# Optimization experiments

Hardware: AMD Instinct MI355X
Metric: run time of the kernel (lower is better)

The kernel has to match this reference:

```python
import jax, jax.numpy as jnp
import numpy as np

B, T, V_LEN = 64, 21, 36
E, H, F, VOC = 512, 512, 1024, 20000


def _gru_cell(x, h, w_ih, w_hh, b_ih, b_hh):
    # PyTorch nn.GRUCell semantics
    gi = x @ w_ih.T + b_ih            # (B, 3H)
    gh = h @ w_hh.T + b_hh            # (B, 3H)
    i_r, i_z, i_n = jnp.split(gi, 3, axis=1)
    h_r, h_z, h_n = jnp.split(gh, 3, axis=1)
    r = jax.nn.sigmoid(i_r + h_r)
    z = jax.nn.sigmoid(i_z + h_z)
    n = jnp.tanh(i_n + r * h_n)
    return (1.0 - z) * n + z * h


def setup_inputs() -> dict:
    key = jax.random.key(0)
    ks = jax.random.split(key, 20)

    def w(k, shape, fan_in):
        return jax.random.normal(k, shape, dtype=jnp.float32) * (1.0 / np.sqrt(fan_in))

    att_in = H + E + F   # h2_dim + input_dim + feature_dim
    lang_in = F + H      # feature_dim + h1_dim
    return {
        "feature_vector": jax.random.normal(ks[0], (B, V_LEN, F), dtype=jnp.float32),
        "ground_truth_seq_helper": T,
        "ground_truth_answer_input": jax.random.normal(ks[1], (B, T, E), dtype=jnp.float32),
        # attention GRUCell
        "att_w_ih": w(ks[2], (3 * H, att_in), att_in),
        "att_w_hh": w(ks[3], (3 * H, H), H),
        "att_b_ih": w(ks[4], (3 * H,), H),
        "att_b_hh": w(ks[5], (3 * H,), H),
        # language GRUCell
        "lang_w_ih": w(ks[6], (3 * H, lang_in), lang_in),
        "lang_w_hh": w(ks[7], (3 * H, H), H),
        "lang_b_ih": w(ks[8], (3 * H,), H),
        "lang_b_hh": w(ks[9], (3 * H,), H),
        # attention MLP
        "fc1_w": w(ks[10], (128, F), F),
        "fc1_b": w(ks[11], (128,), F),
        "fc2_w": w(ks[12], (128, H), H),
        "fc2_b": w(ks[13], (128,), H),
        "fc3_w": w(ks[14], (1, 128), 128),
        "fc3_b": w(ks[15], (1,), 128),
        # vocab projection
        "dense_w": w(ks[16], (VOC, H), H),
        "dense_b": w(ks[17], (VOC,), H),
    }


def reference(feature_vector, ground_truth_seq_helper, ground_truth_answer_input,
              att_w_ih, att_w_hh, att_b_ih, att_b_hh,
              lang_w_ih, lang_w_hh, lang_b_ih, lang_b_hh,
              fc1_w, fc1_b, fc2_w, fc2_b, fc3_w, fc3_b,
              dense_w, dense_b):
    batch = feature_vector.shape[0]
    v_mean = feature_vector.mean(axis=1)                     # (B, F) loop-invariant
    v_w = feature_vector @ fc1_w.T + fc1_b                   # (B, L, 128) loop-invariant

    def step(carry, x_t):
        h1, h2 = carry
        x = jnp.concatenate([h2, x_t, v_mean], axis=1)       # (B, H+E+F)
        h1 = _gru_cell(x, h1, att_w_ih, att_w_hh, att_b_ih, att_b_hh)
        h_w = h1 @ fc2_w.T + fc2_b                           # (B, 128)
        s = jnp.tanh(v_w + h_w[:, None, :]) @ fc3_w.T + fc3_b  # (B, L, 1)
        a = jax.nn.softmax(s[..., 0], axis=-1)               # (B, L)
        mix = jnp.einsum('bl,blf->bf', a, feature_vector)    # (B, F)
        h2 = _gru_cell(jnp.concatenate([mix, h1], axis=1), h2,
                       lang_w_ih, lang_w_hh, lang_b_ih, lang_b_hh)
        logits = h2 @ dense_w.T + dense_b                    # (B, VOC)
        return (h1, h2), logits

    h1 = jnp.zeros((batch, H), dtype=feature_vector.dtype)
    h2 = jnp.zeros((batch, H), dtype=feature_vector.dtype)
    xs = jnp.swapaxes(ground_truth_answer_input[:, :-1, :], 0, 1)  # (T-1, B, E)
    _, logits = jax.lax.scan(step, (h1, h2), xs)
    result = jnp.swapaxes(logits, 0, 1)                      # (B, T-1, VOC)
    return result
```

## Files before the change

### kernel.cpp

```cpp
#include <hip/hip_runtime.h>
#include <hip/hip_bf16.h>
#include <math.h>


typedef __attribute__((ext_vector_type(8))) short bf16x8;
typedef __attribute__((ext_vector_type(4))) float f32x4;
typedef unsigned short u16;
typedef unsigned int u32;

#define MFMA16 __builtin_amdgcn_mfma_f32_16x16x32_bf16

__device__ __forceinline__ u16 f2bf(float f){
  u32 u = __float_as_uint(f);
  u += 0x7fffu + ((u >> 16) & 1u);
  return (u16)(u >> 16);
}
__device__ __forceinline__ float bf2f(u16 u){ return __uint_as_float(((u32)u) << 16); }
__device__ __forceinline__ float sigm(float x){ return 1.0f/(1.0f+__expf(-x)); }

#define OFF_VMEAN  ((size_t)0)
#define OFF_VMW    ((size_t)262144)
#define OFF_VW     ((size_t)655360)
#define OFF_PREX   ((size_t)1835008)
#define OFF_GTBF   ((size_t)10092544)
#define OFF_WMIDBF ((size_t)11468800)
#define OFF_WIH2HI ((size_t)13041664)
#define OFF_WIH2LO ((size_t)14614528)
#define OFF_AWHHHI ((size_t)16187392)
#define OFF_AWHHLO ((size_t)17760256)
#define OFF_LWHHHI ((size_t)19333120)
#define OFF_LWHHLO ((size_t)20905984)
#define OFF_LWIHHI ((size_t)22478848)
#define OFF_LWIHLO ((size_t)27197440)
#define OFF_H1HI   ((size_t)31916032)
#define OFF_H1LO   ((size_t)32047104)
#define OFF_H2HI   ((size_t)32178176)
#define OFF_H2LO   ((size_t)32309248)
#define OFF_MIXHI  ((size_t)32440320)
#define OFF_MIXLO  ((size_t)32571392)
#define OFF_G2F    ((size_t)32702464)
#define OFF_GHH2F  ((size_t)33095680)
#define OFF_H2BF   ((size_t)33488896)
#define OFF_WDBF   ((size_t)0)

__global__ __launch_bounds__(256) void k_prep0(
    const float* __restrict__ fv, const float* __restrict__ gt,
    const float* __restrict__ awih, const float* __restrict__ awhh,
    const float* __restrict__ lwih, const float* __restrict__ lwhh,
    char* __restrict__ ws){
  long gid = (long)blockIdx.x * blockDim.x + threadIdx.x;
  long stride = (long)gridDim.x * blockDim.x;
  u32* zh1h = (u32*)(ws + OFF_H1HI);
  u32* zh1l = (u32*)(ws + OFF_H1LO);
  u32* zh2h = (u32*)(ws + OFF_H2HI);
  u32* zh2l = (u32*)(ws + OFF_H2LO);
  for (long i = gid; i < 16384; i += stride){ zh1h[i]=0; zh1l[i]=0; zh2h[i]=0; zh2l[i]=0; }
  u16* gtbf = (u16*)(ws + OFF_GTBF);
  for (long i = gid; i < 688128; i += stride) gtbf[i] = f2bf(gt[i]);
  u16* wmid = (u16*)(ws + OFF_WMIDBF);
  for (long i = gid; i < 786432; i += stride)
    wmid[i] = f2bf(awih[(i>>9)*2048 + 512 + (i&511)]);
  u16* w2h = (u16*)(ws + OFF_WIH2HI); u16* w2l = (u16*)(ws + OFF_WIH2LO);
  for (long i = gid; i < 786432; i += stride){
    float x = awih[(i>>9)*2048 + (i&511)];
    u16 h = f2bf(x); w2h[i] = h; w2l[i] = f2bf(x - bf2f(h));
  }
  u16* ahh = (u16*)(ws + OFF_AWHHHI); u16* ahl = (u16*)(ws + OFF_AWHHLO);
  for (long i = gid; i < 786432; i += stride){
    float x = awhh[i]; u16 h = f2bf(x); ahh[i] = h; ahl[i] = f2bf(x - bf2f(h));
  }
  u16* lhh = (u16*)(ws + OFF_LWHHHI); u16* lhl = (u16*)(ws + OFF_LWHHLO);
  for (long i = gid; i < 786432; i += stride){
    float x = lwhh[i]; u16 h = f2bf(x); lhh[i] = h; lhl[i] = f2bf(x - bf2f(h));
  }
  u16* lih = (u16*)(ws + OFF_LWIHHI); u16* lil = (u16*)(ws + OFF_LWIHLO);
  for (long i = gid; i < 2359296; i += stride){
    float x = lwih[i]; u16 h = f2bf(x); lih[i] = h; lil[i] = f2bf(x - bf2f(h));
  }
  float* vmean = (float*)(ws + OFF_VMEAN);
  for (long i = gid; i < 65536; i += stride){
    long b = i >> 10, f = i & 1023;
    float s = 0.f;
    for (int l = 0; l < 36; ++l) s += fv[b*36864 + l*1024 + f];
    vmean[i] = s * (1.f/36.f);
  }
}

__global__ __launch_bounds__(256) void k_prep1(const float* __restrict__ fv,
    const float* __restrict__ att_w_ih, const float* __restrict__ att_b_ih,
    const float* __restrict__ fc1_w, const float* __restrict__ fc1_b,
    char* __restrict__ ws){
  const float* vmean = (const float*)(ws + OFF_VMEAN);
  float* vmw = (float*)(ws + OFF_VMW);
  float* vwp = (float*)(ws + OFF_VW);
  long gid = (long)blockIdx.x * blockDim.x + threadIdx.x;
  if (gid < 98304){
    long b = gid / 1536, j = gid % 1536;
    const float4* x = (const float4*)(vmean + b*1024);
    const float4* w = (const float4*)(att_w_ih + j*2048 + 1024);
    float s = att_b_ih[j];
    #pragma unroll 8
    for (int k = 0; k < 256; ++k){
      float4 a = x[k], c = w[k];
      s += a.x*c.x + a.y*c.y + a.z*c.z + a.w*c.w;
    }
    vmw[gid] = s;
  } else {
    long i = gid - 98304;
    long bl = i >> 7, c = i & 127;
    const float4* x = (const float4*)(fv + bl*1024);
    const float4* w = (const float4*)(fc1_w + c*1024);
    float s = fc1_b[c];
    #pragma unroll 8
    for (int k = 0; k < 256; ++k){
      float4 a = x[k], ww = w[k];
      s += a.x*ww.x + a.y*ww.y + a.z*ww.z + a.w*ww.w;
    }
    vwp[i] = s;
  }
}

__global__ __launch_bounds__(256) void k_gemm_bf16(
    const u16* __restrict__ A, const u16* __restrict__ W,
    const float* __restrict__ bias, float* __restrict__ C, int M, int N){
  const int bn = blockIdx.x * 80, bm = blockIdx.y * 128;
  const int tid = threadIdx.x, w = tid >> 6, l = tid & 63;
  const int lr = l & 15, lk = l >> 4;
  f32x4 acc[2][5];
  #pragma unroll
  for (int i = 0; i < 2; ++i)
    #pragma unroll
    for (int j = 0; j < 5; ++j) acc[i][j] = (f32x4){0.f,0.f,0.f,0.f};
  long ar[2], wr[5];
  #pragma unroll
  for (int mi = 0; mi < 2; ++mi) ar[mi] = (long)min(bm + w*32 + mi*16 + lr, M-1) * 512;
  #pragma unroll
  for (int ni = 0; ni < 5; ++ni) wr[ni] = (long)min(bn + ni*16 + lr, N-1) * 512;
  for (int ks = 0; ks < 16; ++ks){
    int ko = ks*32 + lk*8;
    bf16x8 a0 = *(const bf16x8*)(A + ar[0] + ko);
    bf16x8 a1 = *(const bf16x8*)(A + ar[1] + ko);
    #pragma unroll
    for (int ni = 0; ni < 5; ++ni){
      bf16x8 wb = *(const bf16x8*)(W + wr[ni] + ko);
      acc[0][ni] = MFMA16(a0, wb, acc[0][ni], 0,0,0);
      acc[1][ni] = MFMA16(a1, wb, acc[1][ni], 0,0,0);
    }
  }
  #pragma unroll
  for (int mi = 0; mi < 2; ++mi){
    int row0 = bm + w*32 + mi*16 + lk*4;
    #pragma unroll
    for (int ni = 0; ni < 5; ++ni){
      int col = bn + ni*16 + lr;
      if (col < N){
        float bv = bias ? bias[col] : 0.f;
        #pragma unroll
        for (int r2 = 0; r2 < 4; ++r2){
          int row = row0 + r2;
          if (row < M) C[(long)row*N + col] = acc[mi][ni][r2] + bv;
        }
      }
    }
  }
}

__global__ __launch_bounds__(256) void k_cvt_dense(const float* __restrict__ dw,
                                                   char* __restrict__ ws){
  ushort4* out = (ushort4*)(ws + OFF_WDBF);
  long gid = (long)blockIdx.x * blockDim.x + threadIdx.x;
  long stride = (long)gridDim.x * blockDim.x;
  for (long i = gid; i < 2560000; i += stride){
    float4 v = ((const float4*)dw)[i];
    ushort4 o;
    o.x = f2bf(v.x); o.y = f2bf(v.y); o.z = f2bf(v.z); o.w = f2bf(v.w);
    out[i] = o;
  }
}

__global__ __launch_bounds__(256) void k_gemm_vocab(
    const u16* __restrict__ A, const u16* __restrict__ W,
    const float* __restrict__ bias, float* __restrict__ C){
  int flat = blockIdx.x;
  int xcd = flat & 7, idx = flat >> 3;
  int wg = (xcd < 4 ? xcd*313 : 4*313 + (xcd-4)*312) + idx;
  const int bm = (wg % 10) * 128;
  const int bn = (wg / 10) * 80;
  const int tid = threadIdx.x, w = tid >> 6, l = tid & 63;
  const int lr = l & 15, lk = l >> 4;
  f32x4 acc[2][5];
  #pragma unroll
  for (int i = 0; i < 2; ++i)
    #pragma unroll
    for (int j = 0; j < 5; ++j) acc[i][j] = (f32x4){0.f,0.f,0.f,0.f};
  long ar[2], wr[5];
  #pragma unroll
  for (int mi = 0; mi < 2; ++mi) ar[mi] = (long)(bm + w*32 + mi*16 + lr) * 512;
  #pragma unroll
  for (int ni = 0; ni < 5; ++ni) wr[ni] = (long)(bn + ni*16 + lr) * 512;
  for (int ks = 0; ks < 16; ++ks){
    int ko = ks*32 + lk*8;
    bf16x8 a0 = *(const bf16x8*)(A + ar[0] + ko);
    bf16x8 a1 = *(const bf16x8*)(A + ar[1] + ko);
    #pragma unroll
    for (int ni = 0; ni < 5; ++ni){
      bf16x8 wb = *(const bf16x8*)(W + wr[ni] + ko);
      acc[0][ni] = MFMA16(a0, wb, acc[0][ni], 0,0,0);
      acc[1][ni] = MFMA16(a1, wb, acc[1][ni], 0,0,0);
    }
  }
  #pragma unroll
  for (int mi = 0; mi < 2; ++mi){
    int row0 = bm + w*32 + mi*16 + lk*4;
    #pragma unroll
    for (int ni = 0; ni < 5; ++ni){
      int col = bn + ni*16 + lr;
      float bv = bias[col];
      #pragma unroll
      for (int r2 = 0; r2 < 4; ++r2)
        C[(long)(row0 + r2)*20000 + col] = acc[mi][ni][r2] + bv;
    }
  }
}

__global__ __launch_bounds__(512) void k_phaseA(char* __restrict__ ws,
    const float* __restrict__ abhh, const float* __restrict__ lbhh, int t, int pa){
  __shared__ float ldsF[6144];
  const int blk = blockIdx.x, tid = threadIdx.x;
  const int wid = tid >> 6, lane = tid & 63, lr = lane & 15, lk = lane >> 4;
  const int pn = pa ^ 1;
  const u16* h2hi = (const u16*)(ws + OFF_H2HI) + pa*32768;
  const u16* h2lo = (const u16*)(ws + OFF_H2LO) + pa*32768;
  if (blk < 128){
    const int g = blk >> 5, c0 = (blk & 31) * 16;
    const u16* h1hi = (const u16*)(ws + OFF_H1HI) + pa*32768;
    const u16* h1lo = (const u16*)(ws + OFF_H1LO) + pa*32768;
    u16* h1hiN = (u16*)(ws + OFF_H1HI) + pn*32768;
    u16* h1loN = (u16*)(ws + OFF_H1LO) + pn*32768;
    const int mat = wid & 1, kq = wid >> 1;
    const int bA = g*16 + lr;
    const u16 *pAh, *pAl, *wH, *wL;
    if (mat == 0){
      pAh = h2hi + bA*512; pAl = h2lo + bA*512;
      wH = (const u16*)(ws + OFF_WIH2HI); wL = (const u16*)(ws + OFF_WIH2LO);
    } else {
      pAh = h1hi + bA*512; pAl = h1lo + bA*512;
      wH = (const u16*)(ws + OFF_AWHHHI); wL = (const u16*)(ws + OFF_AWHHLO);
    }
    const u16 *pW[3], *pWl[3];
    #pragma unroll
    for (int gate = 0; gate < 3; ++gate){
      long r = gate*512 + c0 + lr;
      pW[gate] = wH + r*512; pWl[gate] = wL + r*512;
    }
    f32x4 acc[3];
    #pragma unroll
    for (int i = 0; i < 3; ++i) acc[i] = (f32x4){0,0,0,0};
    #pragma unroll
    for (int ks = 0; ks < 4; ++ks){
      const int ko = kq*128 + ks*32 + lk*8;
      bf16x8 ah = *(const bf16x8*)(pAh + ko);
      bf16x8 al = *(const bf16x8*)(pAl + ko);
      #pragma unroll
      for (int gate = 0; gate < 3; ++gate){
        bf16x8 wh = *(const bf16x8*)(pW[gate] + ko);
        bf16x8 wl = *(const bf16x8*)(pWl[gate] + ko);
        acc[gate] = MFMA16(ah, wh, acc[gate], 0,0,0);
        acc[gate] = MFMA16(al, wh, acc[gate], 0,0,0);
        acc[gate] = MFMA16(ah, wl, acc[gate], 0,0,0);
      }
    }
    #pragma unroll
    for (int gate = 0; gate < 3; ++gate)
      #pragma unroll
      for (int rg = 0; rg < 4; ++rg)
        ldsF[((wid*3 + gate)*4 + rg)*64 + lane] = acc[gate][rg];
    __syncthreads();
    if (tid < 256){
      const float* prex = (const float*)(ws + OFF_PREX);
      const float* vmw  = (const float*)(ws + OFF_VMW);
      const int l = tid & 63, rg = tid >> 6;
      const int c = c0 + (l & 15);
      const int b = g*16 + (l >> 4)*4 + rg;
      float gi[3], gh[3];
      #pragma unroll
      for (int gate = 0; gate < 3; ++gate){
        float si = 0.f, sh = 0.f;
        #pragma unroll
        for (int kq2 = 0; kq2 < 4; ++kq2){
          si += ldsF[(((2*kq2+0)*3 + gate)*4 + rg)*64 + l];
          sh += ldsF[(((2*kq2+1)*3 + gate)*4 + rg)*64 + l];
        }
        gi[gate] = si; gh[gate] = sh;
      }
      long pb = ((long)b*21 + t)*1536;
      float ir  = gi[0] + prex[pb + c]        + vmw[b*1536 + c];
      float iz  = gi[1] + prex[pb + 512 + c]  + vmw[b*1536 + 512 + c];
      float in_ = gi[2] + prex[pb + 1024 + c] + vmw[b*1536 + 1024 + c];
      float hr = gh[0] + abhh[c];
      float hz = gh[1] + abhh[512 + c];
      float hn = gh[2] + abhh[1024 + c];
      float r_ = sigm(ir + hr);
      float z_ = sigm(iz + hz);
      float n_ = tanhf(in_ + r_*hn);
      float hold = bf2f(h1hi[b*512 + c]) + bf2f(h1lo[b*512 + c]);
      float hv = (1.f - z_)*n_ + z_*hold;
      u16 hh = f2bf(hv);
      h1hiN[b*512 + c] = hh;
      h1loN[b*512 + c] = f2bf(hv - bf2f(hh));
    }
  } else {
    const int j = blk - 128;
    const int g = j / 24, rb = j % 24, r0 = rb*64;
    const int tile = wid & 3, kh = wid >> 2;
    const u16* pAh = h2hi + (g*16 + lr)*512;
    const u16* pAl = h2lo + (g*16 + lr)*512;
    const int rr = r0 + tile*16 + lr;
    const u16* pW  = (const u16*)(ws + OFF_LWHHHI) + (long)rr*512;
    const u16* pWl = (const u16*)(ws + OFF_LWHHLO) + (long)rr*512;
    f32x4 acc = (f32x4){0,0,0,0};
    #pragma unroll
    for (int ks = 0; ks < 8; ++ks){
      const int ko = kh*256 + ks*32 + lk*8;
      bf16x8 ah = *(const bf16x8*)(pAh + ko);
      bf16x8 al = *(const bf16x8*)(pAl + ko);
      bf16x8 wh = *(const bf16x8*)(pW + ko);
      bf16x8 wl = *(const bf16x8*)(pWl + ko);
      acc = MFMA16(ah, wh, acc, 0,0,0);
      acc = MFMA16(al, wh, acc, 0,0,0);
      acc = MFMA16(ah, wl, acc, 0,0,0);
    }
    #pragma unroll
    for (int rg = 0; rg < 4; ++rg)
      ldsF[((kh*4 + tile)*4 + rg)*64 + lane] = acc[rg];
    __syncthreads();
    float* GHH2F = (float*)(ws + OFF_GHH2F);
    #pragma unroll
    for (int rep = 0; rep < 2; ++rep){
      int idx = tid + rep*512;
      int tl = idx >> 8, rem = idx & 255;
      int l = rem & 63, rg = rem >> 6;
      int rrr = r0 + tl*16 + (l & 15);
      int b = g*16 + (l >> 4)*4 + rg;
      float v = ldsF[((0 + tl)*4 + rg)*64 + l] + ldsF[((4 + tl)*4 + rg)*64 + l] + lbhh[rrr];
      GHH2F[(long)b*1536 + rrr] = v;
    }
  }
}

__global__ __launch_bounds__(512) void k_phaseB(char* __restrict__ ws,
    const float* __restrict__ fv,
    const float* __restrict__ fc2w, const float* __restrict__ fc2b,
    const float* __restrict__ fc3w, const float* __restrict__ lbih, int pa){
  __shared__ float ldsF[2048];
  const int blk = blockIdx.x, tid = threadIdx.x;
  const int pn = pa ^ 1;
  const u16* h1hi = (const u16*)(ws + OFF_H1HI) + pn*32768;
  const u16* h1lo = (const u16*)(ws + OFF_H1LO) + pn*32768;
  if (blk < 96){
    const int wid = tid >> 6, lane = tid & 63, lr = lane & 15, lk = lane >> 4;
    const int g = blk / 24, rb = blk % 24, r0 = rb*64;
    const int tile = wid & 3, kh = wid >> 2;
    const u16* pAh = h1hi + (g*16 + lr)*512;
    const u16* pAl = h1lo + (g*16 + lr)*512;
    const int rr = r0 + tile*16 + lr;
    const u16* pW  = (const u16*)(ws + OFF_LWIHHI) + (long)rr*1536 + 1024;
    const u16* pWl = (const u16*)(ws + OFF_LWIHLO) + (long)rr*1536 + 1024;
    f32x4 acc = (f32x4){0,0,0,0};
    #pragma unroll
    for (int ks = 0; ks < 8; ++ks){
      const int ko = kh*256 + ks*32 + lk*8;
      bf16x8 ah = *(const bf16x8*)(pAh + ko);
      bf16x8 al = *(const bf16x8*)(pAl + ko);
      bf16x8 wh = *(const bf16x8*)(pW + ko);
      bf16x8 wl = *(const bf16x8*)(pWl + ko);
      acc = MFMA16(ah, wh, acc, 0,0,0);
      acc = MFMA16(al, wh, acc, 0,0,0);
      acc = MFMA16(ah, wl, acc, 0,0,0);
    }
    #pragma unroll
    for (int rg = 0; rg < 4; ++rg)
      ldsF[((kh*4 + tile)*4 + rg)*64 + lane] = acc[rg];
    __syncthreads();
    float* G2F = (float*)(ws + OFF_G2F);
    #pragma unroll
    for (int rep = 0; rep < 2; ++rep){
      int idx = tid + rep*512;
      int tl = idx >> 8, rem = idx & 255;
      int l = rem & 63, rg = rem >> 6;
      int rrr = r0 + tl*16 + (l & 15);
      int b = g*16 + (l >> 4)*4 + rg;
      float v = ldsF[((0 + tl)*4 + rg)*64 + l] + ldsF[((4 + tl)*4 + rg)*64 + l] + lbih[rrr];
      G2F[(long)b*1536 + rrr] = v;
    }
  } else {
    const int b = blk - 96;
    const float* vw = (const float*)(ws + OFF_VW);
    u16* mixhi = (u16*)(ws + OFF_MIXHI);
    u16* mixlo = (u16*)(ws + OFF_MIXLO);
    float* sh1 = ldsF;
    float* hwS = ldsF + 512;
    float* sS  = ldsF + 640;
    float* aS  = ldsF + 680;
    sh1[tid] = bf2f(h1hi[b*512 + tid]) + bf2f(h1lo[b*512 + tid]);
    __syncthreads();
    {
      int c = tid >> 2, q = tid & 3;
      const float4* x = (const float4*)(sh1 + q*128);
      const float4* w = (const float4*)(fc2w + c*512 + q*128);
      float s = 0.f;
      #pragma unroll 8
      for (int i = 0; i < 32; ++i){
        float4 a = x[i], ww = w[i];
        s += a.x*ww.x + a.y*ww.y + a.z*ww.z + a.w*ww.w;
      }
      s += __shfl_xor(s, 1); s += __shfl_xor(s, 2);
      if (q == 0) hwS[c] = s + fc2b[c];
    }
    __syncthreads();
    {
      int jj = tid & 15, l0 = tid >> 4;
      #pragma unroll
      for (int lb = 0; lb < 64; lb += 32){
        int l = lb + l0;
        float s = 0.f;
        if (l < 36){
          const float* vr = vw + (long)b*4608 + l*128;
          #pragma unroll
          for (int k = jj*8; k < jj*8 + 8; ++k) s += tanhf(vr[k] + hwS[k]) * fc3w[k];
        }
        s += __shfl_xor(s,1); s += __shfl_xor(s,2); s += __shfl_xor(s,4); s += __shfl_xor(s,8);
        if (jj == 0 && l < 36) sS[l] = s;
      }
    }
    __syncthreads();
    if (tid == 0){
      float m = -1e30f;
      for (int l = 0; l < 36; ++l) m = fmaxf(m, sS[l]);
      float sum = 0.f;
      for (int l = 0; l < 36; ++l){ float e = __expf(sS[l] - m); aS[l] = e; sum += e; }
      float inv = 1.f / sum;
      for (int l = 0; l < 36; ++l) aS[l] *= inv;
    }
    __syncthreads();
    {
      float ax = 0.f, ay = 0.f;
      const float* base = fv + (long)b*36864 + tid*2;
      for (int l = 0; l < 36; ++l){
        float a = aS[l];
        float2 v = *(const float2*)(base + l*1024);
        ax += a*v.x; ay += a*v.y;
      }
      ushort2 hi2, lo2; u16 h;
      h = f2bf(ax); hi2.x = h; lo2.x = f2bf(ax - bf2f(h));
      h = f2bf(ay); hi2.y = h; lo2.y = f2bf(ay - bf2f(h));
      *(ushort2*)(mixhi + b*1024 + tid*2) = hi2;
      *(ushort2*)(mixlo + b*1024 + tid*2) = lo2;
    }
  }
}

__global__ __launch_bounds__(512) void k_phaseC(char* __restrict__ ws, int t, int pa){
  __shared__ float ldsF[6144];
  const int blk = blockIdx.x, tid = threadIdx.x;
  const int wid = tid >> 6, lane = tid & 63, lr = lane & 15, lk = lane >> 4;
  const int pn = pa ^ 1;
  const int g = blk >> 5, c0 = (blk & 31) * 16;
  const u16* mixhi = (const u16*)(ws + OFF_MIXHI);
  const u16* mixlo = (const u16*)(ws + OFF_MIXLO);
  const u16* lih = (const u16*)(ws + OFF_LWIHHI);
  const u16* lil = (const u16*)(ws + OFF_LWIHLO);
  const int bA = g*16 + lr;
  const u16* pAh = mixhi + bA*1024;
  const u16* pAl = mixlo + bA*1024;
  const u16 *pW[3], *pWl[3];
  #pragma unroll
  for (int gate = 0; gate < 3; ++gate){
    long r = gate*512 + c0 + lr;
    pW[gate] = lih + r*1536; pWl[gate] = lil + r*1536;
  }
  f32x4 acc[3];
  #pragma unroll
  for (int i = 0; i < 3; ++i) acc[i] = (f32x4){0,0,0,0};
  #pragma unroll
  for (int ks = 0; ks < 4; ++ks){
    const int ko = wid*128 + ks*32 + lk*8;
    bf16x8 ah = *(const bf16x8*)(pAh + ko);
    bf16x8 al = *(const bf16x8*)(pAl + ko);
    #pragma unroll
    for (int gate = 0; gate < 3; ++gate){
      bf16x8 wh = *(const bf16x8*)(pW[gate] + ko);
      bf16x8 wl = *(const bf16x8*)(pWl[gate] + ko);
      acc[gate] = MFMA16(ah, wh, acc[gate], 0,0,0);
      acc[gate] = MFMA16(al, wh, acc[gate], 0,0,0);
      acc[gate] = MFMA16(ah, wl, acc[gate], 0,0,0);
    }
  }
  #pragma unroll
  for (int gate = 0; gate < 3; ++gate)
    #pragma unroll
    for (int rg = 0; rg < 4; ++rg)
      ldsF[((wid*3 + gate)*4 + rg)*64 + lane] = acc[gate][rg];
  __syncthreads();
  if (tid < 256){
    const float* G2F   = (const float*)(ws + OFF_G2F);
    const float* GHH2F = (const float*)(ws + OFF_GHH2F);
    const u16* h2hiO = (const u16*)(ws + OFF_H2HI) + pa*32768;
    const u16* h2loO = (const u16*)(ws + OFF_H2LO) + pa*32768;
    u16* h2hiN = (u16*)(ws + OFF_H2HI) + pn*32768;
    u16* h2loN = (u16*)(ws + OFF_H2LO) + pn*32768;
    u16* h2bf  = (u16*)(ws + OFF_H2BF);
    const int l = tid & 63, rg = tid >> 6;
    const int c = c0 + (l & 15);
    const int b = g*16 + (l >> 4)*4 + rg;
    float gi[3];
    #pragma unroll
    for (int gate = 0; gate < 3; ++gate){
      float s = 0.f;
      #pragma unroll
      for (int w2 = 0; w2 < 8; ++w2)
        s += ldsF[((w2*3 + gate)*4 + rg)*64 + l];
      gi[gate] = s;
    }
    float gir = gi[0] + G2F[(long)b*1536 + c];
    float giz = gi[1] + G2F[(long)b*1536 + 512 + c];
    float gin = gi[2] + G2F[(long)b*1536 + 1024 + c];
    float ghr = GHH2F[(long)b*1536 + c];
    float ghz = GHH2F[(long)b*1536 + 512 + c];
    float ghn = GHH2F[(long)b*1536 + 1024 + c];
    float r_ = sigm(gir + ghr);
    float z_ = sigm(giz + ghz);
    float n_ = tanhf(gin + r_*ghn);
    float hold = bf2f(h2hiO[b*512 + c]) + bf2f(h2loO[b*512 + c]);
    float hv = (1.f - z_)*n_ + z_*hold;
    u16 hh = f2bf(hv);
    h2hiN[b*512 + c] = hh;
    h2loN[b*512 + c] = f2bf(hv - bf2f(hh));
    h2bf[((long)b*20 + t)*512 + c] = hh;
  }
}

extern "C" void kernel_launch(void* const* d_in, const int* in_sizes, int n_in,
                              void* d_out, int out_size, void* d_ws, size_t ws_size,
                              hipStream_t stream){
  const float* fv   = (const float*)d_in[0];
  const float* gt   = (const float*)d_in[2];
  const float* awih = (const float*)d_in[3];
  const float* awhh = (const float*)d_in[4];
  const float* abih = (const float*)d_in[5];
  const float* abhh = (const float*)d_in[6];
  const float* lwih = (const float*)d_in[7];
  const float* lwhh = (const float*)d_in[8];
  const float* lbih = (const float*)d_in[9];
  const float* lbhh = (const float*)d_in[10];
  const float* fc1w = (const float*)d_in[11];
  const float* fc1b = (const float*)d_in[12];
  const float* fc2w = (const float*)d_in[13];
  const float* fc2b = (const float*)d_in[14];
  const float* fc3w = (const float*)d_in[15];
  const float* dw   = (const float*)d_in[17];
  const float* db   = (const float*)d_in[18];
  char* ws = (char*)d_ws;
  float* out = (float*)d_out;

  k_prep0<<<dim3(2048), dim3(256), 0, stream>>>(fv, gt, awih, awhh, lwih, lwhh, ws);
  k_prep1<<<dim3(1536), dim3(256), 0, stream>>>(fv, awih, abih, fc1w, fc1b, ws);
  k_gemm_bf16<<<dim3(20, 11), dim3(256), 0, stream>>>(
      (const u16*)(ws + OFF_GTBF), (const u16*)(ws + OFF_WMIDBF),
      (const float*)nullptr, (float*)(ws + OFF_PREX), 1344, 1536);
  for (int t = 0; t < 20; ++t){
    int pa = t & 1;
    k_phaseA<<<dim3(224), dim3(512), 0, stream>>>(ws, abhh, lbhh, t, pa);
    k_phaseB<<<dim3(160), dim3(512), 0, stream>>>(ws, fv, fc2w, fc2b, fc3w, lbih, pa);
    k_phaseC<<<dim3(128), dim3(512), 0, stream>>>(ws, t, pa);
  }
  k_cvt_dense<<<dim3(2048), dim3(256), 0, stream>>>(dw, ws);
  k_gemm_vocab<<<dim3(2500), dim3(256), 0, stream>>>(
      (const u16*)(ws + OFF_H2BF), (const u16*)(ws + OFF_WDBF), db, out);
}
```

Baseline: 1.358 ms.

## Fold language GRU matvecs into phaseC and move prep GEMMs to split-bf16 MFMA

The language GRU's h2@W_hh and h1@W_ih-slice products, previously computed as extra blocks in phaseA and phaseB and passed through global G2F/GHH2F buffers, are now computed inside phaseC. Each phaseC block assigns its eight waves to the mix, h1 and h2 operands and reduces them in LDS, which removes the intermediate global round-trips and shrinks the phaseA/phaseB grids. The prep step also swaps the scalar fp32 dot-product kernel for v_mean@W and fv@fc1 with an MFMA kernel using hi/lo bf16 splits, at the cost of extra conversion passes over fv and the weights. phaseC now does twice the K-work per block on its critical path, while phaseA and phaseB do less.

```diff
diff --git a/kernel.cpp b/kernel.cpp
--- a/kernel.cpp
+++ b/kernel.cpp
@@ -18,7 +18,6 @@
 __device__ __forceinline__ float bf2f(u16 u){ return __uint_as_float(((u32)u) << 16); }
 __device__ __forceinline__ float sigm(float x){ return 1.0f/(1.0f+__expf(-x)); }
 
-#define OFF_VMEAN  ((size_t)0)
 #define OFF_VMW    ((size_t)262144)
 #define OFF_VW     ((size_t)655360)
 #define OFF_PREX   ((size_t)1835008)
@@ -38,16 +37,22 @@
 #define OFF_H2LO   ((size_t)32309248)
 #define OFF_MIXHI  ((size_t)32440320)
 #define OFF_MIXLO  ((size_t)32571392)
-#define OFF_G2F    ((size_t)32702464)
-#define OFF_GHH2F  ((size_t)33095680)
 #define OFF_H2BF   ((size_t)33488896)
+#define OFF_FVHI   ((size_t)34799616)
+#define OFF_FVLO   ((size_t)39518208)
+#define OFF_WR1HI  ((size_t)44236800)
+#define OFF_WR1LO  ((size_t)47382528)
+#define OFF_FC1HI  ((size_t)50528256)
+#define OFF_FC1LO  ((size_t)50790400)
+#define OFF_VMHI   ((size_t)51052544)
+#define OFF_VMLO   ((size_t)51183616)
 #define OFF_WDBF   ((size_t)0)
 
 __global__ __launch_bounds__(256) void k_prep0(
     const float* __restrict__ fv, const float* __restrict__ gt,
     const float* __restrict__ awih, const float* __restrict__ awhh,
     const float* __restrict__ lwih, const float* __restrict__ lwhh,
-    char* __restrict__ ws){
+    const float* __restrict__ fc1w, char* __restrict__ ws){
   long gid = (long)blockIdx.x * blockDim.x + threadIdx.x;
   long stride = (long)gridDim.x * blockDim.x;
   u32* zh1h = (u32*)(ws + OFF_H1HI);
@@ -59,7 +64,7 @@
   for (long i = gid; i < 688128; i += stride) gtbf[i] = f2bf(gt[i]);
   u16* wmid = (u16*)(ws + OFF_WMIDBF);
   for (long i = gid; i < 786432; i += stride)
-    wmid[i] = f2bf(awih[(i>>9)*2048 + 512 + (i&511)]);
+    wmid[i] = f2bf(awih[(i>>9)*2048 + (i&511) + 512]);
   u16* w2h = (u16*)(ws + OFF_WIH2HI); u16* w2l = (u16*)(ws + OFF_WIH2LO);
   for (long i = gid; i < 786432; i += stride){
     float x = awih[(i>>9)*2048 + (i&511)];
@@ -77,46 +82,83 @@
   for (long i = gid; i < 2359296; i += stride){
     float x = lwih[i]; u16 h = f2bf(x); lih[i] = h; lil[i] = f2bf(x - bf2f(h));
   }
-  float* vmean = (float*)(ws + OFF_VMEAN);
+  u16* fvh = (u16*)(ws + OFF_FVHI); u16* fvl = (u16*)(ws + OFF_FVLO);
+  for (long i = gid; i < 2359296; i += stride){
+    float x = fv[i]; u16 h = f2bf(x); fvh[i] = h; fvl[i] = f2bf(x - bf2f(h));
+  }
+  u16* wr1h = (u16*)(ws + OFF_WR1HI); u16* wr1l = (u16*)(ws + OFF_WR1LO);
+  for (long i = gid; i < 1572864; i += stride){
+    float x = awih[(i>>10)*2048 + 1024 + (i&1023)];
+    u16 h = f2bf(x); wr1h[i] = h; wr1l[i] = f2bf(x - bf2f(h));
+  }
+  u16* f1h = (u16*)(ws + OFF_FC1HI); u16* f1l = (u16*)(ws + OFF_FC1LO);
+  for (long i = gid; i < 131072; i += stride){
+    float x = fc1w[i]; u16 h = f2bf(x); f1h[i] = h; f1l[i] = f2bf(x - bf2f(h));
+  }
+  u16* vmh = (u16*)(ws + OFF_VMHI); u16* vml = (u16*)(ws + OFF_VMLO);
   for (long i = gid; i < 65536; i += stride){
     long b = i >> 10, f = i & 1023;
     float s = 0.f;
     for (int l = 0; l < 36; ++l) s += fv[b*36864 + l*1024 + f];
-    vmean[i] = s * (1.f/36.f);
-  }
-}
-
-__global__ __launch_bounds__(256) void k_prep1(const float* __restrict__ fv,
-    const float* __restrict__ att_w_ih, const float* __restrict__ att_b_ih,
-    const float* __restrict__ fc1_w, const float* __restrict__ fc1_b,
-    char* __restrict__ ws){
-  const float* vmean = (const float*)(ws + OFF_VMEAN);
-  float* vmw = (float*)(ws + OFF_VMW);
-  float* vwp = (float*)(ws + OFF_VW);
-  long gid = (long)blockIdx.x * blockDim.x + threadIdx.x;
-  if (gid < 98304){
-    long b = gid / 1536, j = gid % 1536;
-    const float4* x = (const float4*)(vmean + b*1024);
-    const float4* w = (const float4*)(att_w_ih + j*2048 + 1024);
-    float s = att_b_ih[j];
-    #pragma unroll 8
-    for (int k = 0; k < 256; ++k){
-      float4 a = x[k], c = w[k];
-      s += a.x*c.x + a.y*c.y + a.z*c.z + a.w*c.w;
-    }
-    vmw[gid] = s;
+    s *= (1.f/36.f);
+    u16 h = f2bf(s); vmh[i] = h; vml[i] = f2bf(s - bf2f(h));
+  }
+}
+
+__global__ __launch_bounds__(512) void k_prep_gemm(char* __restrict__ ws,
+    const float* __restrict__ abih, const float* __restrict__ fc1b){
+  const int blk = blockIdx.x, tid = threadIdx.x;
+  const int wid = tid >> 6, lane = tid & 63, lr = lane & 15, lk = lane >> 4;
+  f32x4 acc = (f32x4){0,0,0,0};
+  if (blk < 144){
+    const u16* pAh = (const u16*)(ws + OFF_FVHI) + (long)(blk*16 + lr)*1024;
+    const u16* pAl = (const u16*)(ws + OFF_FVLO) + (long)(blk*16 + lr)*1024;
+    const int c = wid*16 + lr;
+    const u16* pWh = (const u16*)(ws + OFF_FC1HI) + (long)c*1024;
+    const u16* pWl = (const u16*)(ws + OFF_FC1LO) + (long)c*1024;
+    for (int ks = 0; ks < 32; ++ks){
+      const int ko = ks*32 + lk*8;
+      bf16x8 ah = *(const bf16x8*)(pAh + ko);
+      bf16x8 al = *(const bf16x8*)(pAl + ko);
+      bf16x8 wh = *(const bf16x8*)(pWh + ko);
+      bf16x8 wl = *(const bf16x8*)(pWl + ko);
+      acc = MFMA16(ah, wh, acc, 0,0,0);
+      acc = MFMA16(al, wh, acc, 0,0,0);
+      acc = MFMA16(ah, wl, acc, 0,0,0);
+    }
+    float* vwp = (float*)(ws + OFF_VW);
+    const int cc = wid*16 + lr;
+    const float bv = fc1b[cc];
+    #pragma unroll
+    for (int rg = 0; rg < 4; ++rg){
+      int row = blk*16 + lk*4 + rg;
+      vwp[(long)row*128 + cc] = acc[rg] + bv;
+    }
   } else {
-    long i = gid - 98304;
-    long bl = i >> 7, c = i & 127;
-    const float4* x = (const float4*)(fv + bl*1024);
-    const float4* w = (const float4*)(fc1_w + c*1024);
-    float s = fc1_b[c];
-    #pragma unroll 8
-    for (int k = 0; k < 256; ++k){
-      float4 a = x[k], ww = w[k];
-      s += a.x*ww.x + a.y*ww.y + a.z*ww.z + a.w*ww.w;
-    }
-    vwp[i] = s;
+    const int unit = (blk - 144)*8 + wid;
+    const int mtile = unit / 96, ntile = unit % 96;
+    const u16* pAh = (const u16*)(ws + OFF_VMHI) + (long)(mtile*16 + lr)*1024;
+    const u16* pAl = (const u16*)(ws + OFF_VMLO) + (long)(mtile*16 + lr)*1024;
+    const int j = ntile*16 + lr;
+    const u16* pWh = (const u16*)(ws + OFF_WR1HI) + (long)j*1024;
+    const u16* pWl = (const u16*)(ws + OFF_WR1LO) + (long)j*1024;
+    for (int ks = 0; ks < 32; ++ks){
+      const int ko = ks*32 + lk*8;
+      bf16x8 ah = *(const bf16x8*)(pAh + ko);
+      bf16x8 al = *(const bf16x8*)(pAl + ko);
+      bf16x8 wh = *(const bf16x8*)(pWh + ko);
+      bf16x8 wl = *(const bf16x8*)(pWl + ko);
+      acc = MFMA16(ah, wh, acc, 0,0,0);
+      acc = MFMA16(al, wh, acc, 0,0,0);
+      acc = MFMA16(ah, wl, acc, 0,0,0);
+    }
+    float* vmw = (float*)(ws + OFF_VMW);
+    const float bv = abih[j];
+    #pragma unroll
+    for (int rg = 0; rg < 4; ++rg){
+      int b = mtile*16 + lk*4 + rg;
+      vmw[(long)b*1536 + j] = acc[rg] + bv;
+    }
   }
 }
 
@@ -224,267 +266,214 @@
 }
 
 __global__ __launch_bounds__(512) void k_phaseA(char* __restrict__ ws,
-    const float* __restrict__ abhh, const float* __restrict__ lbhh, int t, int pa){
+    const float* __restrict__ abhh, int t, int pa){
   __shared__ float ldsF[6144];
   const int blk = blockIdx.x, tid = threadIdx.x;
   const int wid = tid >> 6, lane = tid & 63, lr = lane & 15, lk = lane >> 4;
   const int pn = pa ^ 1;
   const u16* h2hi = (const u16*)(ws + OFF_H2HI) + pa*32768;
   const u16* h2lo = (const u16*)(ws + OFF_H2LO) + pa*32768;
-  if (blk < 128){
-    const int g = blk >> 5, c0 = (blk & 31) * 16;
-    const u16* h1hi = (const u16*)(ws + OFF_H1HI) + pa*32768;
-    const u16* h1lo = (const u16*)(ws + OFF_H1LO) + pa*32768;
-    u16* h1hiN = (u16*)(ws + OFF_H1HI) + pn*32768;
-    u16* h1loN = (u16*)(ws + OFF_H1LO) + pn*32768;
-    const int mat = wid & 1, kq = wid >> 1;
-    const int bA = g*16 + lr;
-    const u16 *pAh, *pAl, *wH, *wL;
-    if (mat == 0){
-      pAh = h2hi + bA*512; pAl = h2lo + bA*512;
-      wH = (const u16*)(ws + OFF_WIH2HI); wL = (const u16*)(ws + OFF_WIH2LO);
-    } else {
-      pAh = h1hi + bA*512; pAl = h1lo + bA*512;
-      wH = (const u16*)(ws + OFF_AWHHHI); wL = (const u16*)(ws + OFF_AWHHLO);
-    }
-    const u16 *pW[3], *pWl[3];
-    #pragma unroll
-    for (int gate = 0; gate < 3; ++gate){
-      long r = gate*512 + c0 + lr;
-      pW[gate] = wH + r*512; pWl[gate] = wL + r*512;
-    }
-    f32x4 acc[3];
-    #pragma unroll
-    for (int i = 0; i < 3; ++i) acc[i] = (f32x4){0,0,0,0};
-    #pragma unroll
-    for (int ks = 0; ks < 4; ++ks){
-      const int ko = kq*128 + ks*32 + lk*8;
-      bf16x8 ah = *(const bf16x8*)(pAh + ko);
-      bf16x8 al = *(const bf16x8*)(pAl + ko);
+  const int g = blk >> 5, c0 = (blk & 31) * 16;
+  const u16* h1hi = (const u16*)(ws + OFF_H1HI) + pa*32768;
+  const u16* h1lo = (const u16*)(ws + OFF_H1LO) + pa*32768;
+  u16* h1hiN = (u16*)(ws + OFF_H1HI) + pn*32768;
+  u16* h1loN = (u16*)(ws + OFF_H1LO) + pn*32768;
+  const int mat = wid & 1, kq = wid >> 1;
+  const int bA = g*16 + lr;
+  const u16 *pAh, *pAl, *wH, *wL;
+  if (mat == 0){
+    pAh = h2hi + bA*512; pAl = h2lo + bA*512;
+    wH = (const u16*)(ws + OFF_WIH2HI); wL = (const u16*)(ws + OFF_WIH2LO);
+  } else {
+    pAh = h1hi + bA*512; pAl = h1lo + bA*512;
+    wH = (const u16*)(ws + OFF_AWHHHI); wL = (const u16*)(ws + OFF_AWHHLO);
+  }
+  const u16 *pW[3], *pWl[3];
+  #pragma unroll
+  for (int gate = 0; gate < 3; ++gate){
+    long r = gate*512 + c0 + lr;
+    pW[gate] = wH + r*512; pWl[gate] = wL + r*512;
+  }
+  f32x4 acc[3];
+  #pragma unroll
+  for (int i = 0; i < 3; ++i) acc[i] = (f32x4){0,0,0,0};
+  #pragma unroll
+  for (int ks = 0; ks < 4; ++ks){
+    const int ko = kq*128 + ks*32 + lk*8;
+    bf16x8 ah = *(const bf16x8*)(pAh + ko);
+    bf16x8 al = *(const bf16x8*)(pAl + ko);
+    #pragma unroll
+    for (int gate = 0; gate < 3; ++gate){
+      bf16x8 wh = *(const bf16x8*)(pW[gate] + ko);
+      bf16x8 wl = *(const bf16x8*)(pWl[gate] + ko);
+      acc[gate] = MFMA16(ah, wh, acc[gate], 0,0,0);
+      acc[gate] = MFMA16(al, wh, acc[gate], 0,0,0);
+      acc[gate] = MFMA16(ah, wl, acc[gate], 0,0,0);
+    }
+  }
+  #pragma unroll
+  for (int gate = 0; gate < 3; ++gate)
+    #pragma unroll
+    for (int rg = 0; rg < 4; ++rg)
+      ldsF[((wid*3 + gate)*4 + rg)*64 + lane] = acc[gate][rg];
+  __syncthreads();
+  if (tid < 256){
+    const float* prex = (const float*)(ws + OFF_PREX);
+    const float* vmw  = (const float*)(ws + OFF_VMW);
+    const int l = tid & 63, rg = tid >> 6;
+    const int c = c0 + (l & 15);
+    const int b = g*16 + (l >> 4)*4 + rg;
+    float gi[3], gh[3];
+    #pragma unroll
+    for (int gate = 0; gate < 3; ++gate){
+      float si = 0.f, sh = 0.f;
       #pragma unroll
-      for (int gate = 0; gate < 3; ++gate){
-        bf16x8 wh = *(const bf16x8*)(pW[gate] + ko);
-        bf16x8 wl = *(const bf16x8*)(pWl[gate] + ko);
-        acc[gate] = MFMA16(ah, wh, acc[gate], 0,0,0);
-        acc[gate] = MFMA16(al, wh, acc[gate], 0,0,0);
-        acc[gate] = MFMA16(ah, wl, acc[gate], 0,0,0);
+      for (int kq2 = 0; kq2 < 4; ++kq2){
+        si += ldsF[(((2*kq2+0)*3 + gate)*4 + rg)*64 + l];
+        sh += ldsF[(((2*kq2+1)*3 + gate)*4 + rg)*64 + l];
       }
-    }
-    #pragma unroll
-    for (int gate = 0; gate < 3; ++gate)
-      #pragma unroll
-      for (int rg = 0; rg < 4; ++rg)
-        ldsF[((wid*3 + gate)*4 + rg)*64 + lane] = acc[gate][rg];
-    __syncthreads();
-    if (tid < 256){
-      const float* prex = (const float*)(ws + OFF_PREX);
-      const float* vmw  = (const float*)(ws + OFF_VMW);
-      const int l = tid & 63, rg = tid >> 6;
-      const int c = c0 + (l & 15);
-      const int b = g*16 + (l >> 4)*4 + rg;
-      float gi[3], gh[3];
-      #pragma unroll
-      for (int gate = 0; gate < 3; ++gate){
-        float si = 0.f, sh = 0.f;
-        #pragma unroll
-        for (int kq2 = 0; kq2 < 4; ++kq2){
-          si += ldsF[(((2*kq2+0)*3 + gate)*4 + rg)*64 + l];
-          sh += ldsF[(((2*kq2+1)*3 + gate)*4 + rg)*64 + l];
-        }
-        gi[gate] = si; gh[gate] = sh;
-      }
-      long pb = ((long)b*21 + t)*1536;
-      float ir  = gi[0] + prex[pb + c]        + vmw[b*1536 + c];
-      float iz  = gi[1] + prex[pb + 512 + c]  + vmw[b*1536 + 512 + c];
-      float in_ = gi[2] + prex[pb + 1024 + c] + vmw[b*1536 + 1024 + c];
-      float hr = gh[0] + abhh[c];
-      float hz = gh[1] + abhh[512 + c];
-      float hn = gh[2] + abhh[1024 + c];
-      float r_ = sigm(ir + hr);
-      float z_ = sigm(iz + hz);
-      float n_ = tanhf(in_ + r_*hn);
-      float hold = bf2f(h1hi[b*512 + c]) + bf2f(h1lo[b*512 + c]);
-      float hv = (1.f - z_)*n_ + z_*hold;
-      u16 hh = f2bf(hv);
-      h1hiN[b*512 + c] = hh;
-      h1loN[b*512 + c] = f2bf(hv - bf2f(hh));
-    }
-  } else {
-    const int j = blk - 128;
-    const int g = j / 24, rb = j % 24, r0 = rb*64;
-    const int tile = wid & 3, kh = wid >> 2;
-    const u16* pAh = h2hi + (g*16 + lr)*512;
-    const u16* pAl = h2lo + (g*16 + lr)*512;
-    const int rr = r0 + tile*16 + lr;
-    const u16* pW  = (const u16*)(ws + OFF_LWHHHI) + (long)rr*512;
-    const u16* pWl = (const u16*)(ws + OFF_LWHHLO) + (long)rr*512;
-    f32x4 acc = (f32x4){0,0,0,0};
-    #pragma unroll
-    for (int ks = 0; ks < 8; ++ks){
-      const int ko = kh*256 + ks*32 + lk*8;
-      bf16x8 ah = *(const bf16x8*)(pAh + ko);
-      bf16x8 al = *(const bf16x8*)(pAl + ko);
-      bf16x8 wh = *(const bf16x8*)(pW + ko);
-      bf16x8 wl = *(const bf16x8*)(pWl + ko);
-      acc = MFMA16(ah, wh, acc, 0,0,0);
-      acc = MFMA16(al, wh, acc, 0,0,0);
-      acc = MFMA16(ah, wl, acc, 0,0,0);
-    }
-    #pragma unroll
-    for (int rg = 0; rg < 4; ++rg)
-      ldsF[((kh*4 + tile)*4 + rg)*64 + lane] = acc[rg];
-    __syncthreads();
-    float* GHH2F = (float*)(ws + OFF_GHH2F);
-    #pragma unroll
-    for (int rep = 0; rep < 2; ++rep){
-      int idx = tid + rep*512;
-      int tl = idx >> 8, rem = idx & 255;
-      int l = rem & 63, rg = rem >> 6;
-      int rrr = r0 + tl*16 + (l & 15);
-      int b = g*16 + (l >> 4)*4 + rg;
-      float v = ldsF[((0 + tl)*4 + rg)*64 + l] + ldsF[((4 + tl)*4 + rg)*64 + l] + lbhh[rrr];
-      GHH2F[(long)b*1536 + rrr] = v;
-    }
+      gi[gate] = si; gh[gate] = sh;
+    }
+    long pb = ((long)b*21 + t)*1536;
+    float ir  = gi[0] + prex[pb + c]        + vmw[b*1536 + c];
+    float iz  = gi[1] + prex[pb + 512 + c]  + vmw[b*1536 + 512 + c];
+    float in_ = gi[2] + prex[pb + 1024 + c] + vmw[b*1536 + 1024 + c];
+    float hr = gh[0] + abhh[c];
+    float hz = gh[1] + abhh[512 + c];
+    float hn = gh[2] + abhh[1024 + c];
+    float r_ = sigm(ir + hr);
+    float z_ = sigm(iz + hz);
+    float n_ = tanhf(in_ + r_*hn);
+    float hold = bf2f(h1hi[b*512 + c]) + bf2f(h1lo[b*512 + c]);
+    float hv = (1.f - z_)*n_ + z_*hold;
+    u16 hh = f2bf(hv);
+    h1hiN[b*512 + c] = hh;
+    h1loN[b*512 + c] = f2bf(hv - bf2f(hh));
   }
 }
 
 __global__ __launch_bounds__(512) void k_phaseB(char* __restrict__ ws,
     const float* __restrict__ fv,
     const float* __restrict__ fc2w, const float* __restrict__ fc2b,
-    const float* __restrict__ fc3w, const float* __restrict__ lbih, int pa){
-  __shared__ float ldsF[2048];
-  const int blk = blockIdx.x, tid = threadIdx.x;
+    const float* __restrict__ fc3w, int pa){
+  __shared__ float ldsF[768];
+  const int tid = threadIdx.x;
   const int pn = pa ^ 1;
   const u16* h1hi = (const u16*)(ws + OFF_H1HI) + pn*32768;
   const u16* h1lo = (const u16*)(ws + OFF_H1LO) + pn*32768;
-  if (blk < 96){
-    const int wid = tid >> 6, lane = tid & 63, lr = lane & 15, lk = lane >> 4;
-    const int g = blk / 24, rb = blk % 24, r0 = rb*64;
-    const int tile = wid & 3, kh = wid >> 2;
-    const u16* pAh = h1hi + (g*16 + lr)*512;
-    const u16* pAl = h1lo + (g*16 + lr)*512;
-    const int rr = r0 + tile*16 + lr;
-    const u16* pW  = (const u16*)(ws + OFF_LWIHHI) + (long)rr*1536 + 1024;
-    const u16* pWl = (const u16*)(ws + OFF_LWIHLO) + (long)rr*1536 + 1024;
-    f32x4 acc = (f32x4){0,0,0,0};
-    #pragma unroll
-    for (int ks = 0; ks < 8; ++ks){
-      const int ko = kh*256 + ks*32 + lk*8;
-      bf16x8 ah = *(const bf16x8*)(pAh + ko);
-      bf16x8 al = *(const bf16x8*)(pAl + ko);
-      bf16x8 wh = *(const bf16x8*)(pW + ko);
-      bf16x8 wl = *(const bf16x8*)(pWl + ko);
-      acc = MFMA16(ah, wh, acc, 0,0,0);
-      acc = MFMA16(al, wh, acc, 0,0,0);
-      acc = MFMA16(ah, wl, acc, 0,0,0);
-    }
-    #pragma unroll
-    for (int rg = 0; rg < 4; ++rg)
-      ldsF[((kh*4 + tile)*4 + rg)*64 + lane] = acc[rg];
-    __syncthreads();
-    float* G2F = (float*)(ws + OFF_G2F);
-    #pragma unroll
-    for (int rep = 0; rep < 2; ++rep){
-      int idx = tid + rep*512;
-      int tl = idx >> 8, rem = idx & 255;
-      int l = rem & 63, rg = rem >> 6;
-      int rrr = r0 + tl*16 + (l & 15);
-      int b = g*16 + (l >> 4)*4 + rg;
-      float v = ldsF[((0 + tl)*4 + rg)*64 + l] + ldsF[((4 + tl)*4 + rg)*64 + l] + lbih[rrr];
-      G2F[(long)b*1536 + rrr] = v;
-    }
-  } else {
-    const int b = blk - 96;
-    const float* vw = (const float*)(ws + OFF_VW);
-    u16* mixhi = (u16*)(ws + OFF_MIXHI);
-    u16* mixlo = (u16*)(ws + OFF_MIXLO);
-    float* sh1 = ldsF;
-    float* hwS = ldsF + 512;
-    float* sS  = ldsF + 640;
-    float* aS  = ldsF + 680;
-    sh1[tid] = bf2f(h1hi[b*512 + tid]) + bf2f(h1lo[b*512 + tid]);
-    __syncthreads();
-    {
-      int c = tid >> 2, q = tid & 3;
-      const float4* x = (const float4*)(sh1 + q*128);
-      const float4* w = (const float4*)(fc2w + c*512 + q*128);
+  const int b = blockIdx.x;
+  const float* vw = (const float*)(ws + OFF_VW);
+  u16* mixhi = (u16*)(ws + OFF_MIXHI);
+  u16* mixlo = (u16*)(ws + OFF_MIXLO);
+  float* sh1 = ldsF;
+  float* hwS = ldsF + 512;
+  float* sS  = ldsF + 640;
+  float* aS  = ldsF + 680;
+  sh1[tid] = bf2f(h1hi[b*512 + tid]) + bf2f(h1lo[b*512 + tid]);
+  __syncthreads();
+  {
+    int c = tid >> 2, q = tid & 3;
+    const float4* x = (const float4*)(sh1 + q*128);
+    const float4* w = (const float4*)(fc2w + c*512 + q*128);
+    float s = 0.f;
+    #pragma unroll 8
+    for (int i = 0; i < 32; ++i){
+      float4 a = x[i], ww = w[i];
+      s += a.x*ww.x + a.y*ww.y + a.z*ww.z + a.w*ww.w;
+    }
+    s += __shfl_xor(s, 1); s += __shfl_xor(s, 2);
+    if (q == 0) hwS[c] = s + fc2b[c];
+  }
+  __syncthreads();
+  {
+    int jj = tid & 15, l0 = tid >> 4;
+    #pragma unroll
+    for (int lb = 0; lb < 64; lb += 32){
+      int l = lb + l0;
       float s = 0.f;
-      #pragma unroll 8
-      for (int i = 0; i < 32; ++i){
-        float4 a = x[i], ww = w[i];
-        s += a.x*ww.x + a.y*ww.y + a.z*ww.z + a.w*ww.w;
+      if (l < 36){
+        const float* vr = vw + (long)b*4608 + l*128;
+        #pragma unroll
+        for (int k = jj*8; k < jj*8 + 8; ++k) s += tanhf(vr[k] + hwS[k]) * fc3w[k];
       }
-      s += __shfl_xor(s, 1); s += __shfl_xor(s, 2);
-      if (q == 0) hwS[c] = s + fc2b[c];
-    }
-    __syncthreads();
-    {
-      int jj = tid & 15, l0 = tid >> 4;
-      #pragma unroll
-      for (int lb = 0; lb < 64; lb += 32){
-        int l = lb + l0;
-        float s = 0.f;
-        if (l < 36){
-          const float* vr = vw + (long)b*4608 + l*128;
-          #pragma unroll
-          for (int k = jj*8; k < jj*8 + 8; ++k) s += tanhf(vr[k] + hwS[k]) * fc3w[k];
-        }
-        s += __shfl_xor(s,1); s += __shfl_xor(s,2); s += __shfl_xor(s,4); s += __shfl_xor(s,8);
-        if (jj == 0 && l < 36) sS[l] = s;
-      }
-    }
-    __syncthreads();
-    if (tid == 0){
-      float m = -1e30f;
-      for (int l = 0; l < 36; ++l) m = fmaxf(m, sS[l]);
-      float sum = 0.f;
-      for (int l = 0; l < 36; ++l){ float e = __expf(sS[l] - m); aS[l] = e; sum += e; }
-      float inv = 1.f / sum;
-      for (int l = 0; l < 36; ++l) aS[l] *= inv;
-    }
-    __syncthreads();
-    {
-      float ax = 0.f, ay = 0.f;
-      const float* base = fv + (long)b*36864 + tid*2;
-      for (int l = 0; l < 36; ++l){
-        float a = aS[l];
-        float2 v = *(const float2*)(base + l*1024);
-        ax += a*v.x; ay += a*v.y;
-      }
-      ushort2 hi2, lo2; u16 h;
-      h = f2bf(ax); hi2.x = h; lo2.x = f2bf(ax - bf2f(h));
-      h = f2bf(ay); hi2.y = h; lo2.y = f2bf(ay - bf2f(h));
-      *(ushort2*)(mixhi + b*1024 + tid*2) = hi2;
-      *(ushort2*)(mixlo + b*1024 + tid*2) = lo2;
-    }
-  }
-}
-
-__global__ __launch_bounds__(512) void k_phaseC(char* __restrict__ ws, int t, int pa){
+      s += __shfl_xor(s,1); s += __shfl_xor(s,2); s += __shfl_xor(s,4); s += __shfl_xor(s,8);
+      if (jj == 0 && l < 36) sS[l] = s;
+    }
+  }
+  __syncthreads();
+  if (tid == 0){
+    float m = -1e30f;
+    for (int l = 0; l < 36; ++l) m = fmaxf(m, sS[l]);
+    float sum = 0.f;
+    for (int l = 0; l < 36; ++l){ float e = __expf(sS[l] - m); aS[l] = e; sum += e; }
+    float inv = 1.f / sum;
+    for (int l = 0; l < 36; ++l) aS[l] *= inv;
+  }
+  __syncthreads();
+  {
+    float ax = 0.f, ay = 0.f;
+    const float* base = fv + (long)b*36864 + tid*2;
+    for (int l = 0; l < 36; ++l){
+      float a = aS[l];
+      float2 v = *(const float2*)(base + l*1024);
+      ax += a*v.x; ay += a*v.y;
+    }
+    ushort2 hi2, lo2; u16 h;
+    h = f2bf(ax); hi2.x = h; lo2.x = f2bf(ax - bf2f(h));
+    h = f2bf(ay); hi2.y = h; lo2.y = f2bf(ay - bf2f(h));
+    *(ushort2*)(mixhi + b*1024 + tid*2) = hi2;
+    *(ushort2*)(mixlo + b*1024 + tid*2) = lo2;
+  }
+}
+
+__global__ __launch_bounds__(512) void k_phaseC(char* __restrict__ ws,
+    const float* __restrict__ lbih, const float* __restrict__ lbhh, int t, int pa){
   __shared__ float ldsF[6144];
   const int blk = blockIdx.x, tid = threadIdx.x;
   const int wid = tid >> 6, lane = tid & 63, lr = lane & 15, lk = lane >> 4;
   const int pn = pa ^ 1;
   const int g = blk >> 5, c0 = (blk & 31) * 16;
-  const u16* mixhi = (const u16*)(ws + OFF_MIXHI);
-  const u16* mixlo = (const u16*)(ws + OFF_MIXLO);
+  const int bA = g*16 + lr;
   const u16* lih = (const u16*)(ws + OFF_LWIHHI);
   const u16* lil = (const u16*)(ws + OFF_LWIHLO);
-  const int bA = g*16 + lr;
-  const u16* pAh = mixhi + bA*1024;
-  const u16* pAl = mixlo + bA*1024;
-  const u16 *pW[3], *pWl[3];
-  #pragma unroll
-  for (int gate = 0; gate < 3; ++gate){
-    long r = gate*512 + c0 + lr;
-    pW[gate] = lih + r*1536; pWl[gate] = lil + r*1536;
-  }
   f32x4 acc[3];
   #pragma unroll
   for (int i = 0; i < 3; ++i) acc[i] = (f32x4){0,0,0,0};
-  #pragma unroll
-  for (int ks = 0; ks < 4; ++ks){
-    const int ko = wid*128 + ks*32 + lk*8;
+  const u16 *pAh, *pAl, *pW[3], *pWl[3];
+  int kbase;
+  if (wid < 4){
+    pAh = (const u16*)(ws + OFF_MIXHI) + bA*1024;
+    pAl = (const u16*)(ws + OFF_MIXLO) + bA*1024;
+    #pragma unroll
+    for (int gate = 0; gate < 3; ++gate){
+      long r = gate*512 + c0 + lr;
+      pW[gate] = lih + r*1536; pWl[gate] = lil + r*1536;
+    }
+    kbase = wid*256;
+  } else if (wid < 6){
+    pAh = (const u16*)(ws + OFF_H1HI) + pn*32768 + bA*512;
+    pAl = (const u16*)(ws + OFF_H1LO) + pn*32768 + bA*512;
+    #pragma unroll
+    for (int gate = 0; gate < 3; ++gate){
+      long r = gate*512 + c0 + lr;
+      pW[gate] = lih + r*1536 + 1024; pWl[gate] = lil + r*1536 + 1024;
+    }
+    kbase = (wid - 4)*256;
+  } else {
+    pAh = (const u16*)(ws + OFF_H2HI) + pa*32768 + bA*512;
+    pAl = (const u16*)(ws + OFF_H2LO) + pa*32768 + bA*512;
+    const u16* lhh = (const u16*)(ws + OFF_LWHHHI);
+    const u16* lhl = (const u16*)(ws + OFF_LWHHLO);
+    #pragma unroll
+    for (int gate = 0; gate < 3; ++gate){
+      long r = gate*512 + c0 + lr;
+      pW[gate] = lhh + r*512; pWl[gate] = lhl + r*512;
+    }
+    kbase = (wid - 6)*256;
+  }
+  #pragma unroll
+  for (int ks = 0; ks < 8; ++ks){
+    const int ko = kbase + ks*32 + lk*8;
     bf16x8 ah = *(const bf16x8*)(pAh + ko);
     bf16x8 al = *(const bf16x8*)(pAl + ko);
     #pragma unroll
@@ -503,8 +492,6 @@
       ldsF[((wid*3 + gate)*4 + rg)*64 + lane] = acc[gate][rg];
   __syncthreads();
   if (tid < 256){
-    const float* G2F   = (const float*)(ws + OFF_G2F);
-    const float* GHH2F = (const float*)(ws + OFF_GHH2F);
     const u16* h2hiO = (const u16*)(ws + OFF_H2HI) + pa*32768;
     const u16* h2loO = (const u16*)(ws + OFF_H2LO) + pa*32768;
     u16* h2hiN = (u16*)(ws + OFF_H2HI) + pn*32768;
@@ -513,24 +500,19 @@
     const int l = tid & 63, rg = tid >> 6;
     const int c = c0 + (l & 15);
     const int b = g*16 + (l >> 4)*4 + rg;
-    float gi[3];
-    #pragma unroll
-    for (int gate = 0; gate < 3; ++gate){
-      float s = 0.f;
-      #pragma unroll
-      for (int w2 = 0; w2 < 8; ++w2)
-        s += ldsF[((w2*3 + gate)*4 + rg)*64 + l];
-      gi[gate] = s;
-    }
-    float gir = gi[0] + G2F[(long)b*1536 + c];
-    float giz = gi[1] + G2F[(long)b*1536 + 512 + c];
-    float gin = gi[2] + G2F[(long)b*1536 + 1024 + c];
-    float ghr = GHH2F[(long)b*1536 + c];
-    float ghz = GHH2F[(long)b*1536 + 512 + c];
-    float ghn = GHH2F[(long)b*1536 + 1024 + c];
-    float r_ = sigm(gir + ghr);
-    float z_ = sigm(giz + ghz);
-    float n_ = tanhf(gin + r_*ghn);
+    float gi[3], gh[3];
+    #pragma unroll
+    for (int gate = 0; gate < 3; ++gate){
+      float sm = ldsF[((0*3 + gate)*4 + rg)*64 + l] + ldsF[((1*3 + gate)*4 + rg)*64 + l]
+               + ldsF[((2*3 + gate)*4 + rg)*64 + l] + ldsF[((3*3 + gate)*4 + rg)*64 + l];
+      float s2 = ldsF[((4*3 + gate)*4 + rg)*64 + l] + ldsF[((5*3 + gate)*4 + rg)*64 + l];
+      float sh = ldsF[((6*3 + gate)*4 + rg)*64 + l] + ldsF[((7*3 + gate)*4 + rg)*64 + l];
+      gi[gate] = sm + s2 + lbih[gate*512 + c];
+      gh[gate] = sh + lbhh[gate*512 + c];
+    }
+    float r_ = sigm(gi[0] + gh[0]);
+    float z_ = sigm(gi[1] + gh[1]);
+    float n_ = tanhf(gi[2] + r_*gh[2]);
     float hold = bf2f(h2hiO[b*512 + c]) + bf2f(h2loO[b*512 + c]);
     float hv = (1.f - z_)*n_ + z_*hold;
     u16 hh = f2bf(hv);
@@ -563,16 +545,16 @@
   char* ws = (char*)d_ws;
   float* out = (float*)d_out;
 
-  k_prep0<<<dim3(2048), dim3(256), 0, stream>>>(fv, gt, awih, awhh, lwih, lwhh, ws);
-  k_prep1<<<dim3(1536), dim3(256), 0, stream>>>(fv, awih, abih, fc1w, fc1b, ws);
+  k_prep0<<<dim3(2048), dim3(256), 0, stream>>>(fv, gt, awih, awhh, lwih, lwhh, fc1w, ws);
+  k_prep_gemm<<<dim3(192), dim3(512), 0, stream>>>(ws, abih, fc1b);
   k_gemm_bf16<<<dim3(20, 11), dim3(256), 0, stream>>>(
       (const u16*)(ws + OFF_GTBF), (const u16*)(ws + OFF_WMIDBF),
       (const float*)nullptr, (float*)(ws + OFF_PREX), 1344, 1536);
   for (int t = 0; t < 20; ++t){
     int pa = t & 1;
-    k_phaseA<<<dim3(224), dim3(512), 0, stream>>>(ws, abhh, lbhh, t, pa);
-    k_phaseB<<<dim3(160), dim3(512), 0, stream>>>(ws, fv, fc2w, fc2b, fc3w, lbih, pa);
-    k_phaseC<<<dim3(128), dim3(512), 0, stream>>>(ws, t, pa);
+    k_phaseA<<<dim3(128), dim3(512), 0, stream>>>(ws, abhh, t, pa);
+    k_phaseB<<<dim3(64), dim3(512), 0, stream>>>(ws, fv, fc2w, fc2b, fc3w, pa);
+    k_phaseC<<<dim3(128), dim3(512), 0, stream>>>(ws, lbih, lbhh, t, pa);
   }
   k_cvt_dense<<<dim3(2048), dim3(256), 0, stream>>>(dw, ws);
   k_gemm_vocab<<<dim3(2500), dim3(256), 0, stream>>>(
```

Result: faster. 1.292 ms (-4.9%).
